# Kernel optimization log

Measured on AMD Instinct MI355X. Metric: run time of the kernel, lower is better.

The kernel has to match this reference:

```python
import jax, jax.numpy as jnp
import numpy as np

B, S, NGB, NG, DIM = 64, 4096, 13, 48, 3
NCH = [8, 8, 1]
NSHELLS = 8


def setup_inputs() -> dict:
    key = jax.random.key(0)
    ks = jax.random.split(key, 16)
    rng = np.random.default_rng(0)
    # valid row-wise permutations of the N_ngb neighbor slots per group op
    GnnPerms = jnp.asarray(np.argsort(rng.random((NG, NGB)), axis=1), dtype=jnp.int64)
    NNSites = jax.random.randint(ks[0], (NGB, S), 0, S, dtype=jnp.int64)
    SitesToShells = jax.random.randint(ks[1], (S,), 0, NSHELLS, dtype=jnp.int64)
    # block-diagonal (Ng*dim, Ng*dim) cartesian rotation blocks
    blk = rng.normal(size=(NG, DIM, DIM)).astype(np.float32) * 0.5
    gd = np.zeros((NG * DIM, NG * DIM), np.float32)
    for g in range(NG):
        gd[g * DIM:(g + 1) * DIM, g * DIM:(g + 1) * DIM] = blk[g]
    gdiags = jnp.asarray(gd)
    std = 0.2
    return {
        "InStates": jax.random.normal(ks[2], (B, 1, S), jnp.float32),
        "Psi0": jax.random.normal(ks[3], (NCH[0], 1, NGB), jnp.float32) * std,
        "bias0": jax.random.normal(ks[4], (NCH[0], 1), jnp.float32) * std,
        "Psi1": jax.random.normal(ks[5], (NCH[1], NCH[0], NGB), jnp.float32) * std,
        "bias1": jax.random.normal(ks[6], (NCH[1], 1), jnp.float32) * std,
        "Psi2": jax.random.normal(ks[7], (NCH[2], NCH[1], NGB), jnp.float32) * std,
        "bias2": jax.random.normal(ks[8], (NCH[2], 1), jnp.float32) * std,
        "wtVC": jax.random.normal(ks[9], (DIM, NGB), jnp.float32) * std,
        "ShellWeights": jax.random.normal(ks[10], (NSHELLS,), jnp.float32) * std,
        "gdiags": gdiags,
        "GnnPerms": GnnPerms,
        "NNSites": NNSites,
        "SitesToShells": SitesToShells,
    }


def _rearrange(x, NNSites):
    # x: (B, Nch, S) -> (B, Nch*N_ngb, S); subchannel j of channel c holds x[b, c, NNSites[j, s]]
    b, c, s = x.shape
    return x[:, :, NNSites].reshape(b, c * NGB, s)


def _gconv(x, W, b):
    # x: (B, NchIn*N_ngb, S); W: (NchOut, NchIn, N_ngb); b: (NchOut, 1)
    # group-rotated weights: GW[o, g, c*N_ngb+j] = W[o, c, GnnPerms[g, j]]
    GW = _gconv.GW_cache  # set per-call below via closure-free pattern; replaced in reference
    raise NotImplementedError


def reference(InStates, Psi0, bias0, Psi1, bias1, Psi2, bias2, wtVC,
              ShellWeights, gdiags, GnnPerms, NNSites, SitesToShells):
    act = jax.nn.softplus

    def gconv(x, W, b):
        # rotated weights: (NchOut, Ng, NchIn*N_ngb)
        GW = W[:, :, GnnPerms].transpose(0, 2, 1, 3).reshape(W.shape[0], NG, -1)
        h = jnp.einsum('ogk,bks->bogs', GW, x) + b[:, :, None]  # (B, NchOut, Ng, S)
        return act(h).mean(axis=2)                               # group-orbit average

    out = _rearrange(InStates, NNSites)
    for W, b in ((Psi0, bias0), (Psi1, bias1), (Psi2, bias2)):
        out = gconv(out, W, b)                 # (B, NchOut, S)
        out = _rearrange(out, NNSites)         # (B, NchOut*N_ngb, S)
    # vector channel: row g*dim+d of P is wtVC[d, GnnPerms[g]]
    P = wtVC[:, GnnPerms].transpose(1, 0, 2).reshape(NG * DIM, NGB)
    Wvc = gdiags @ P                           # (Ng*dim, N_ngb)
    v = jnp.einsum('kn,bns->bks', Wvc, out)    # (B, Ng*dim, S)
    v = v.reshape(-1, NG, DIM, out.shape[-1]).mean(axis=1)  # (B, dim, S)
    v = v * ShellWeights[SitesToShells]        # per-site shell weighting
    return v.sum(axis=2) / out.shape[-1]       # (B, dim)
```

## Files before the change

### kernel.cpp

```cpp
#include <hip/hip_runtime.h>
#include <hip/hip_bf16.h>

#define BATCH 64
#define SITES 4096
#define NGB 13
#define NGRP 48
#define SDIM 3

typedef __bf16 bf16x8 __attribute__((ext_vector_type(8)));
typedef float  f32x4  __attribute__((ext_vector_type(4)));

#define OFF_AVC  0
#define OFF_U    64
#define OFF_A0   67648
#define OFF_A1   2164800
#define OFF_PART 4261952
#define UW0H 0
#define UW0L 12288
#define UW1H 24576
#define UW1L 73728
#define UW2H 122880
#define UW2L 129024

__device__ __forceinline__ float softplus_f(float h) {
    return fmaxf(h, 0.f) + __logf(1.f + __expf(-fabsf(h)));
}

__global__ __launch_bounds__(256) void precompute_kernel(
    const float* __restrict__ Psi0, const float* __restrict__ Psi1,
    const float* __restrict__ Psi2, const float* __restrict__ wtVC,
    const float* __restrict__ gdiags, const int* __restrict__ perms,
    float* __restrict__ ws)
{
    float*  Avc = ws + OFF_AVC;
    __bf16* U   = (__bf16*)(ws + OFF_U);
    int t = blockIdx.x * 256 + threadIdx.x;
    if (t < 12288) {
        int k = t & 31, row = t >> 5;
        int o = row / NGRP, g = row - o * NGRP;
        float w = (k < NGB) ? Psi0[o * NGB + perms[g * NGB + k]] : 0.f;
        __bf16 hi = (__bf16)w;
        U[UW0H + t] = hi;
        U[UW0L + t] = (__bf16)(w - (float)hi);
    } else if (t < 61440) {
        int u = t - 12288;
        int k = u & 127, row = u >> 7;
        int o = row / NGRP, g = row - o * NGRP;
        float w = 0.f;
        if (k < 104) { int j = k >> 3, c = k & 7;
                       w = Psi1[(o * 8 + c) * NGB + perms[g * NGB + j]]; }
        __bf16 hi = (__bf16)w;
        U[UW1H + u] = hi;
        U[UW1L + u] = (__bf16)(w - (float)hi);
    } else if (t < 67584) {
        int u = t - 61440;
        int k = u & 127, g = u >> 7;
        float w = 0.f;
        if (k < 104) { int j = k >> 3, c = k & 7;
                       w = Psi2[c * NGB + perms[g * NGB + j]]; }
        __bf16 hi = (__bf16)w;
        U[UW2H + u] = hi;
        U[UW2L + u] = (__bf16)(w - (float)hi);
    } else if (t < 67584 + 39 * NGRP) {
        int t2 = t - 67584;
        int g = t2 % NGRP, u = t2 / NGRP;
        int d = u / NGB, n = u % NGB;
        const int row = g * SDIM + d;
        float s = 0.f;
        for (int k = 0; k < NGRP * SDIM; k++) {
            int g2 = k / SDIM, d2 = k - g2 * SDIM;
            float p = wtVC[d2 * NGB + perms[g2 * NGB + n]];
            s = fmaf(gdiags[row * (NGRP * SDIM) + k], p, s);
        }
        atomicAdd(&Avc[u], s * (1.f / 48.f));
    }
}

template<int NCIN, int NCTOT, int CT, int KPAD, int KSTR, int NWAVES, int NWN>
__global__ __launch_bounds__(NWAVES * 64) void layer_mfma(
    const float* __restrict__ prev,
    const __bf16* __restrict__ Wh,
    const __bf16* __restrict__ Wl,
    const float* __restrict__ bias,
    const int*   __restrict__ NN,
    float* __restrict__ out)
{
    constexpr int NTHR   = NWAVES * 64;
    constexpr int K      = NCIN * NGB;
    constexpr int M      = NCTOT * NGRP;
    constexpr int MTILES = M / 16, NTILES = CT / 16;
    constexpr int NWM    = NWAVES / NWN;
    constexpr int MT_W   = MTILES / NWM, NT_W = NTILES / NWN;
    constexpr int KT     = KPAD / 32;

    static_assert(MT_W * 16 == NGRP, "wave covers exactly one o");
    static_assert(NWM * MT_W == MTILES && NWN * NT_W == NTILES, "");
    static_assert((KPAD & 31) == 0 && (KSTR & 7) == 0, "");

    __shared__ __bf16 xh_lds[CT * KSTR];
    __shared__ __bf16 xl_lds[CT * KSTR];

    const int tid  = threadIdx.x;
    const int wave = tid >> 6, lane = tid & 63;
    const int m16  = lane & 15, quad = lane >> 4;

    const int b  = blockIdx.x / (SITES / CT);
    const int s0 = (blockIdx.x % (SITES / CT)) * CT;

    if constexpr (NCIN == 1) {
        for (int site = tid; site < NGB * CT; site += NTHR) {
            int j = site / CT, col = site % CT;
            int nn = NN[j * SITES + s0 + col];
            float v = prev[(size_t)b * SITES + nn];
            __bf16 hi = (__bf16)v;
            xh_lds[col * KSTR + j] = hi;
            xl_lds[col * KSTR + j] = (__bf16)(v - (float)hi);
        }
        for (int e = tid; e < CT * (KPAD - NGB); e += NTHR) {
            int col = e / (KPAD - NGB), p = e % (KPAD - NGB);
            xh_lds[col * KSTR + NGB + p] = (__bf16)0.f;
            xl_lds[col * KSTR + NGB + p] = (__bf16)0.f;
        }
    } else {
        for (int site = tid; site < NGB * CT; site += NTHR) {
            int j = site / CT, col = site % CT;
            int nn = NN[j * SITES + s0 + col];
            const float4* p4 = (const float4*)(prev + ((size_t)(b * SITES + nn)) * 8);
            float4 u0 = p4[0], u1 = p4[1];
            float v[8] = {u0.x, u0.y, u0.z, u0.w, u1.x, u1.y, u1.z, u1.w};
            bf16x8 hv, lv;
#pragma unroll
            for (int c = 0; c < 8; c++) {
                __bf16 hi = (__bf16)v[c];
                hv[c] = hi;
                lv[c] = (__bf16)(v[c] - (float)hi);
            }
            *(bf16x8*)(xh_lds + col * KSTR + j * 8) = hv;
            *(bf16x8*)(xl_lds + col * KSTR + j * 8) = lv;
        }
        const bf16x8 z8 = {};
        for (int e = tid; e < CT * 3; e += NTHR) {
            int col = e % CT, z = e / CT;
            *(bf16x8*)(xh_lds + col * KSTR + 104 + z * 8) = z8;
            *(bf16x8*)(xl_lds + col * KSTR + 104 + z * 8) = z8;
        }
    }
    __syncthreads();

    const int wave_mt0 = (wave / NWN) * MT_W;
    const int wave_nt0 = (wave % NWN) * NT_W;
    const int o_g      = (wave_mt0 * 16) / NGRP;

    f32x4 acc[MT_W][NT_W];
#pragma unroll
    for (int mt = 0; mt < MT_W; mt++)
#pragma unroll
        for (int nt = 0; nt < NT_W; nt++) acc[mt][nt] = (f32x4){0.f, 0.f, 0.f, 0.f};

#pragma unroll
    for (int kt = 0; kt < KT; kt++) {
        const int koff = kt * 32 + quad * 8;
        bf16x8 ah[MT_W], al[MT_W], bh[NT_W], bl[NT_W];
#pragma unroll
        for (int mt = 0; mt < MT_W; mt++) {
            int row = (wave_mt0 + mt) * 16 + m16;
            ah[mt] = *(const bf16x8*)(Wh + (size_t)row * KPAD + koff);
            al[mt] = *(const bf16x8*)(Wl + (size_t)row * KPAD + koff);
        }
#pragma unroll
        for (int nt = 0; nt < NT_W; nt++) {
            int cbase = ((wave_nt0 + nt) * 16 + m16) * KSTR + koff;
            bh[nt] = *(const bf16x8*)(xh_lds + cbase);
            bl[nt] = *(const bf16x8*)(xl_lds + cbase);
        }
#pragma unroll
        for (int mt = 0; mt < MT_W; mt++)
#pragma unroll
            for (int nt = 0; nt < NT_W; nt++) {
                acc[mt][nt] = __builtin_amdgcn_mfma_f32_16x16x32_bf16(
                    ah[mt], bh[nt], acc[mt][nt], 0, 0, 0);
                acc[mt][nt] = __builtin_amdgcn_mfma_f32_16x16x32_bf16(
                    al[mt], bh[nt], acc[mt][nt], 0, 0, 0);
                acc[mt][nt] = __builtin_amdgcn_mfma_f32_16x16x32_bf16(
                    ah[mt], bl[nt], acc[mt][nt], 0, 0, 0);
            }
    }

    const float bo = bias[o_g];
#pragma unroll
    for (int nt = 0; nt < NT_W; nt++) {
        float s = 0.f;
#pragma unroll
        for (int mt = 0; mt < MT_W; mt++)
#pragma unroll
            for (int r = 0; r < 4; r++)
                s += softplus_f(acc[mt][nt][r] + bo);
        s += __shfl_xor(s, 16);
        s += __shfl_xor(s, 32);
        if (quad == 0)
            out[((size_t)(b * SITES + s0 + (wave_nt0 + nt) * 16 + m16)) * NCTOT + o_g]
                = s * (1.f / 48.f);
    }
}

__global__ __launch_bounds__(256) void reduce_a(
    const float* __restrict__ A2, const int* __restrict__ NN,
    const int* __restrict__ s2sh, const float* __restrict__ sw,
    const float* __restrict__ Avc, float* __restrict__ partial)
{
    const int b = blockIdx.x >> 4;
    const int chunk = blockIdx.x & 15;
    const int tid = threadIdx.x;
    const int s = (chunk << 8) + tid;
    const float* a = A2 + (size_t)b * SITES;

    float y0 = 0.f, y1 = 0.f, y2 = 0.f;
#pragma unroll
    for (int n = 0; n < NGB; n++) {
        float v = a[NN[n * SITES + s]];
        y0 = fmaf(Avc[n],           v, y0);
        y1 = fmaf(Avc[NGB + n],     v, y1);
        y2 = fmaf(Avc[2 * NGB + n], v, y2);
    }
    const float wgt = sw[s2sh[s]];
    y0 *= wgt; y1 *= wgt; y2 *= wgt;

    __shared__ float red[3][256];
    red[0][tid] = y0; red[1][tid] = y1; red[2][tid] = y2;
    __syncthreads();
    for (int st = 128; st > 0; st >>= 1) {
        if (tid < st) {
            red[0][tid] += red[0][tid + st];
            red[1][tid] += red[1][tid + st];
            red[2][tid] += red[2][tid + st];
        }
        __syncthreads();
    }
    if (tid < 3) partial[(b * 16 + chunk) * 3 + tid] = red[tid][0];
}

__global__ __launch_bounds__(256) void reduce_b(
    const float* __restrict__ partial, float* __restrict__ out)
{
    int t = threadIdx.x;
    if (t < BATCH * 3) {
        int b = t / 3, d = t - b * 3;
        float s = 0.f;
        for (int c = 0; c < 16; c++) s += partial[(b * 16 + c) * 3 + d];
        out[t] = s * (1.f / (float)SITES);
    }
}

extern "C" void kernel_launch(void* const* d_in, const int* in_sizes, int n_in,
                              void* d_out, int out_size, void* d_ws, size_t ws_size,
                              hipStream_t stream)
{
    const float* InStates = (const float*)d_in[0];
    const float* Psi0     = (const float*)d_in[1];
    const float* bias0    = (const float*)d_in[2];
    const float* Psi1     = (const float*)d_in[3];
    const float* bias1    = (const float*)d_in[4];
    const float* Psi2     = (const float*)d_in[5];
    const float* bias2    = (const float*)d_in[6];
    const float* wtVC     = (const float*)d_in[7];
    const float* ShellW   = (const float*)d_in[8];
    const float* gdiags   = (const float*)d_in[9];
    const int*   GnnPerms = (const int*)d_in[10];
    const int*   NNSites  = (const int*)d_in[11];
    const int*   S2Sh     = (const int*)d_in[12];

    float*  ws   = (float*)d_ws;
    float*  Avc  = ws + OFF_AVC;
    __bf16* U    = (__bf16*)(ws + OFF_U);
    float*  A0   = ws + OFF_A0;
    float*  A1   = ws + OFF_A1;
    float*  A2   = ws + OFF_A0;
    float*  PART = ws + OFF_PART;

    float* out = (float*)d_out;

    hipMemsetAsync(Avc, 0, 39 * sizeof(float), stream);
    precompute_kernel<<<272, 256, 0, stream>>>(Psi0, Psi1, Psi2, wtVC, gdiags,
                                               GnnPerms, ws);

    layer_mfma<1, 8, 64, 32, 40, 8, 1><<<BATCH * (SITES / 64), 512, 0, stream>>>(
        InStates, U + UW0H, U + UW0L, bias0, NNSites, A0);
    layer_mfma<8, 8, 64, 128, 136, 8, 1><<<BATCH * (SITES / 64), 512, 0, stream>>>(
        A0, U + UW1H, U + UW1L, bias1, NNSites, A1);
    layer_mfma<8, 1, 64, 128, 136, 4, 4><<<BATCH * (SITES / 64), 256, 0, stream>>>(
        A1, U + UW2H, U + UW2L, bias2, NNSites, A2);

    reduce_a<<<BATCH * 16, 256, 0, stream>>>(A2, NNSites, S2Sh, ShellW, Avc, PART);
    reduce_b<<<1, 256, 0, stream>>>(PART, out);
}
```

Measured before the change: 372.6 us.

## Make layer kernels persistent over site chunks with double-buffered LDS gather prefetch

Each block of the layer kernels now handles 8 consecutive 64-site chunks instead of one. The neighbour gather for the next chunk is issued into registers before the MFMA loop and written to a second LDS buffer afterwards, with NN indices loaded two chunks ahead. This aims to hide gather latency behind MFMA work and to amortise block setup and zero-padding. In exchange it launches 8x fewer blocks, which may reduce parallelism across CUs, adds register pressure for the prefetched data, and doubles LDS use.

```diff
diff --git a/kernel.cpp b/kernel.cpp
--- a/kernel.cpp
+++ b/kernel.cpp
@@ -76,8 +76,9 @@
     }
 }
 
-template<int NCIN, int NCTOT, int CT, int KPAD, int KSTR, int NWAVES, int NWN>
-__global__ __launch_bounds__(NWAVES * 64) void layer_mfma(
+template<int NCIN, int NCTOT, int CT, int KPAD, int KSTR, int NWAVES, int NWN,
+         int CHUNKS>
+__global__ __launch_bounds__(NWAVES * 64, 4) void layer_mfma(
     const float* __restrict__ prev,
     const __bf16* __restrict__ Wh,
     const __bf16* __restrict__ Wl,
@@ -86,120 +87,209 @@
     float* __restrict__ out)
 {
     constexpr int NTHR   = NWAVES * 64;
-    constexpr int K      = NCIN * NGB;
     constexpr int M      = NCTOT * NGRP;
     constexpr int MTILES = M / 16, NTILES = CT / 16;
     constexpr int NWM    = NWAVES / NWN;
     constexpr int MT_W   = MTILES / NWM, NT_W = NTILES / NWN;
     constexpr int KT     = KPAD / 32;
+    constexpr int GS     = NGB * CT;
+    constexpr int SPT    = (GS + NTHR - 1) / NTHR;
+    constexpr int CPB    = SITES / CT;
+    constexpr int BUF    = CT * KSTR;
 
     static_assert(MT_W * 16 == NGRP, "wave covers exactly one o");
     static_assert(NWM * MT_W == MTILES && NWN * NT_W == NTILES, "");
     static_assert((KPAD & 31) == 0 && (KSTR & 7) == 0, "");
-
-    __shared__ __bf16 xh_lds[CT * KSTR];
-    __shared__ __bf16 xl_lds[CT * KSTR];
+    static_assert(CPB % CHUNKS == 0, "block stays within one batch");
+
+    __shared__ __bf16 xh_lds[2 * BUF];
+    __shared__ __bf16 xl_lds[2 * BUF];
 
     const int tid  = threadIdx.x;
     const int wave = tid >> 6, lane = tid & 63;
     const int m16  = lane & 15, quad = lane >> 4;
 
-    const int b  = blockIdx.x / (SITES / CT);
-    const int s0 = (blockIdx.x % (SITES / CT)) * CT;
+    const int chunk0 = blockIdx.x * CHUNKS;
+    const int b      = chunk0 / CPB;
+    const int s0base = (chunk0 % CPB) * CT;
+
+    int sj[SPT], scol[SPT];
+    bool sv[SPT];
+#pragma unroll
+    for (int i = 0; i < SPT; i++) {
+        int site = tid + i * NTHR;
+        sv[i] = (site < GS);
+        int ss = sv[i] ? site : 0;
+        sj[i] = ss / CT;
+        scol[i] = ss % CT;
+    }
 
     if constexpr (NCIN == 1) {
-        for (int site = tid; site < NGB * CT; site += NTHR) {
-            int j = site / CT, col = site % CT;
-            int nn = NN[j * SITES + s0 + col];
+        for (int e = tid; e < 2 * CT * (KPAD - NGB); e += NTHR) {
+            int buf = e / (CT * (KPAD - NGB));
+            int r   = e % (CT * (KPAD - NGB));
+            int col = r / (KPAD - NGB), p = r % (KPAD - NGB);
+            xh_lds[buf * BUF + col * KSTR + NGB + p] = (__bf16)0.f;
+            xl_lds[buf * BUF + col * KSTR + NGB + p] = (__bf16)0.f;
+        }
+    } else {
+        const bf16x8 z8 = {};
+        for (int e = tid; e < 2 * CT * 3; e += NTHR) {
+            int buf = e / (CT * 3);
+            int r   = e % (CT * 3);
+            int col = r % CT, z = r / CT;
+            *(bf16x8*)(xh_lds + buf * BUF + col * KSTR + 104 + z * 8) = z8;
+            *(bf16x8*)(xl_lds + buf * BUF + col * KSTR + 104 + z * 8) = z8;
+        }
+    }
+
+#pragma unroll
+    for (int i = 0; i < SPT; i++) if (sv[i]) {
+        int nn = NN[sj[i] * SITES + s0base + scol[i]];
+        if constexpr (NCIN == 1) {
             float v = prev[(size_t)b * SITES + nn];
             __bf16 hi = (__bf16)v;
-            xh_lds[col * KSTR + j] = hi;
-            xl_lds[col * KSTR + j] = (__bf16)(v - (float)hi);
-        }
-        for (int e = tid; e < CT * (KPAD - NGB); e += NTHR) {
-            int col = e / (KPAD - NGB), p = e % (KPAD - NGB);
-            xh_lds[col * KSTR + NGB + p] = (__bf16)0.f;
-            xl_lds[col * KSTR + NGB + p] = (__bf16)0.f;
-        }
-    } else {
-        for (int site = tid; site < NGB * CT; site += NTHR) {
-            int j = site / CT, col = site % CT;
-            int nn = NN[j * SITES + s0 + col];
+            xh_lds[scol[i] * KSTR + sj[i]] = hi;
+            xl_lds[scol[i] * KSTR + sj[i]] = (__bf16)(v - (float)hi);
+        } else {
             const float4* p4 = (const float4*)(prev + ((size_t)(b * SITES + nn)) * 8);
             float4 u0 = p4[0], u1 = p4[1];
             float v[8] = {u0.x, u0.y, u0.z, u0.w, u1.x, u1.y, u1.z, u1.w};
             bf16x8 hv, lv;
 #pragma unroll
-            for (int c = 0; c < 8; c++) {
-                __bf16 hi = (__bf16)v[c];
-                hv[c] = hi;
-                lv[c] = (__bf16)(v[c] - (float)hi);
-            }
-            *(bf16x8*)(xh_lds + col * KSTR + j * 8) = hv;
-            *(bf16x8*)(xl_lds + col * KSTR + j * 8) = lv;
-        }
-        const bf16x8 z8 = {};
-        for (int e = tid; e < CT * 3; e += NTHR) {
-            int col = e % CT, z = e / CT;
-            *(bf16x8*)(xh_lds + col * KSTR + 104 + z * 8) = z8;
-            *(bf16x8*)(xl_lds + col * KSTR + 104 + z * 8) = z8;
-        }
+            for (int c8 = 0; c8 < 8; c8++) {
+                __bf16 hi = (__bf16)v[c8];
+                hv[c8] = hi;
+                lv[c8] = (__bf16)(v[c8] - (float)hi);
+            }
+            *(bf16x8*)(xh_lds + scol[i] * KSTR + sj[i] * 8) = hv;
+            *(bf16x8*)(xl_lds + scol[i] * KSTR + sj[i] * 8) = lv;
+        }
+    }
+
+    int nnA[SPT];
+    if (CHUNKS > 1) {
+        const int s1 = s0base + CT;
+#pragma unroll
+        for (int i = 0; i < SPT; i++)
+            nnA[i] = sv[i] ? NN[sj[i] * SITES + s1 + scol[i]] : 0;
     }
     __syncthreads();
 
     const int wave_mt0 = (wave / NWN) * MT_W;
     const int wave_nt0 = (wave % NWN) * NT_W;
     const int o_g      = (wave_mt0 * 16) / NGRP;
-
-    f32x4 acc[MT_W][NT_W];
-#pragma unroll
-    for (int mt = 0; mt < MT_W; mt++)
-#pragma unroll
-        for (int nt = 0; nt < NT_W; nt++) acc[mt][nt] = (f32x4){0.f, 0.f, 0.f, 0.f};
-
-#pragma unroll
-    for (int kt = 0; kt < KT; kt++) {
-        const int koff = kt * 32 + quad * 8;
-        bf16x8 ah[MT_W], al[MT_W], bh[NT_W], bl[NT_W];
-#pragma unroll
-        for (int mt = 0; mt < MT_W; mt++) {
-            int row = (wave_mt0 + mt) * 16 + m16;
-            ah[mt] = *(const bf16x8*)(Wh + (size_t)row * KPAD + koff);
-            al[mt] = *(const bf16x8*)(Wl + (size_t)row * KPAD + koff);
-        }
+    const float bo     = bias[o_g];
+
+#pragma unroll 1
+    for (int c = 0; c < CHUNKS; c++) {
+        const int cur = c & 1;
+
+        float4 ga[SPT], gb[SPT];
+        float  g1[SPT];
+        if (c + 1 < CHUNKS) {
+#pragma unroll
+            for (int i = 0; i < SPT; i++) if (sv[i]) {
+                if constexpr (NCIN == 1) {
+                    g1[i] = prev[(size_t)b * SITES + nnA[i]];
+                } else {
+                    const float4* p4 =
+                        (const float4*)(prev + ((size_t)(b * SITES + nnA[i])) * 8);
+                    ga[i] = p4[0];
+                    gb[i] = p4[1];
+                }
+            }
+        }
+        int nnB[SPT];
+        if (c + 2 < CHUNKS) {
+            const int s2 = s0base + (c + 2) * CT;
+#pragma unroll
+            for (int i = 0; i < SPT; i++)
+                nnB[i] = sv[i] ? NN[sj[i] * SITES + s2 + scol[i]] : 0;
+        }
+
+        const __bf16* xh = xh_lds + cur * BUF;
+        const __bf16* xl = xl_lds + cur * BUF;
+
+        f32x4 acc[MT_W][NT_W];
+#pragma unroll
+        for (int mt = 0; mt < MT_W; mt++)
+#pragma unroll
+            for (int nt = 0; nt < NT_W; nt++) acc[mt][nt] = (f32x4){0.f, 0.f, 0.f, 0.f};
+
+#pragma unroll
+        for (int kt = 0; kt < KT; kt++) {
+            const int koff = kt * 32 + quad * 8;
+            bf16x8 ah[MT_W], al[MT_W], bh[NT_W], bl[NT_W];
+#pragma unroll
+            for (int mt = 0; mt < MT_W; mt++) {
+                int row = (wave_mt0 + mt) * 16 + m16;
+                ah[mt] = *(const bf16x8*)(Wh + (size_t)row * KPAD + koff);
+                al[mt] = *(const bf16x8*)(Wl + (size_t)row * KPAD + koff);
+            }
+#pragma unroll
+            for (int nt = 0; nt < NT_W; nt++) {
+                int cbase = ((wave_nt0 + nt) * 16 + m16) * KSTR + koff;
+                bh[nt] = *(const bf16x8*)(xh + cbase);
+                bl[nt] = *(const bf16x8*)(xl + cbase);
+            }
+#pragma unroll
+            for (int mt = 0; mt < MT_W; mt++)
+#pragma unroll
+                for (int nt = 0; nt < NT_W; nt++) {
+                    acc[mt][nt] = __builtin_amdgcn_mfma_f32_16x16x32_bf16(
+                        ah[mt], bh[nt], acc[mt][nt], 0, 0, 0);
+                    acc[mt][nt] = __builtin_amdgcn_mfma_f32_16x16x32_bf16(
+                        al[mt], bh[nt], acc[mt][nt], 0, 0, 0);
+                    acc[mt][nt] = __builtin_amdgcn_mfma_f32_16x16x32_bf16(
+                        ah[mt], bl[nt], acc[mt][nt], 0, 0, 0);
+                }
+        }
+
+        const int s0c = s0base + c * CT;
 #pragma unroll
         for (int nt = 0; nt < NT_W; nt++) {
-            int cbase = ((wave_nt0 + nt) * 16 + m16) * KSTR + koff;
-            bh[nt] = *(const bf16x8*)(xh_lds + cbase);
-            bl[nt] = *(const bf16x8*)(xl_lds + cbase);
-        }
-#pragma unroll
-        for (int mt = 0; mt < MT_W; mt++)
-#pragma unroll
-            for (int nt = 0; nt < NT_W; nt++) {
-                acc[mt][nt] = __builtin_amdgcn_mfma_f32_16x16x32_bf16(
-                    ah[mt], bh[nt], acc[mt][nt], 0, 0, 0);
-                acc[mt][nt] = __builtin_amdgcn_mfma_f32_16x16x32_bf16(
-                    al[mt], bh[nt], acc[mt][nt], 0, 0, 0);
-                acc[mt][nt] = __builtin_amdgcn_mfma_f32_16x16x32_bf16(
-                    ah[mt], bl[nt], acc[mt][nt], 0, 0, 0);
-            }
-    }
-
-    const float bo = bias[o_g];
-#pragma unroll
-    for (int nt = 0; nt < NT_W; nt++) {
-        float s = 0.f;
-#pragma unroll
-        for (int mt = 0; mt < MT_W; mt++)
-#pragma unroll
-            for (int r = 0; r < 4; r++)
-                s += softplus_f(acc[mt][nt][r] + bo);
-        s += __shfl_xor(s, 16);
-        s += __shfl_xor(s, 32);
-        if (quad == 0)
-            out[((size_t)(b * SITES + s0 + (wave_nt0 + nt) * 16 + m16)) * NCTOT + o_g]
-                = s * (1.f / 48.f);
+            float s = 0.f;
+#pragma unroll
+            for (int mt = 0; mt < MT_W; mt++)
+#pragma unroll
+                for (int r = 0; r < 4; r++)
+                    s += softplus_f(acc[mt][nt][r] + bo);
+            s += __shfl_xor(s, 16);
+            s += __shfl_xor(s, 32);
+            if (quad == 0)
+                out[((size_t)(b * SITES + s0c + (wave_nt0 + nt) * 16 + m16)) * NCTOT + o_g]
+                    = s * (1.f / 48.f);
+        }
+
+        if (c + 1 < CHUNKS) {
+            __bf16* dh = xh_lds + (cur ^ 1) * BUF;
+            __bf16* dl = xl_lds + (cur ^ 1) * BUF;
+#pragma unroll
+            for (int i = 0; i < SPT; i++) if (sv[i]) {
+                if constexpr (NCIN == 1) {
+                    float v = g1[i];
+                    __bf16 hi = (__bf16)v;
+                    dh[scol[i] * KSTR + sj[i]] = hi;
+                    dl[scol[i] * KSTR + sj[i]] = (__bf16)(v - (float)hi);
+                } else {
+                    float v[8] = {ga[i].x, ga[i].y, ga[i].z, ga[i].w,
+                                  gb[i].x, gb[i].y, gb[i].z, gb[i].w};
+                    bf16x8 hv, lv;
+#pragma unroll
+                    for (int c8 = 0; c8 < 8; c8++) {
+                        __bf16 hi = (__bf16)v[c8];
+                        hv[c8] = hi;
+                        lv[c8] = (__bf16)(v[c8] - (float)hi);
+                    }
+                    *(bf16x8*)(dh + scol[i] * KSTR + sj[i] * 8) = hv;
+                    *(bf16x8*)(dl + scol[i] * KSTR + sj[i] * 8) = lv;
+                }
+            }
+#pragma unroll
+            for (int i = 0; i < SPT; i++) nnA[i] = nnB[i];
+        }
+        __syncthreads();
     }
 }
 
@@ -283,11 +373,14 @@
     precompute_kernel<<<272, 256, 0, stream>>>(Psi0, Psi1, Psi2, wtVC, gdiags,
                                                GnnPerms, ws);
 
-    layer_mfma<1, 8, 64, 32, 40, 8, 1><<<BATCH * (SITES / 64), 512, 0, stream>>>(
+    constexpr int CHUNKS = 8;
+    constexpr int NBLK   = BATCH * (SITES / 64) / CHUNKS;
+
+    layer_mfma<1, 8, 64, 32, 40, 8, 1, CHUNKS><<<NBLK, 512, 0, stream>>>(
         InStates, U + UW0H, U + UW0L, bias0, NNSites, A0);
-    layer_mfma<8, 8, 64, 128, 136, 8, 1><<<BATCH * (SITES / 64), 512, 0, stream>>>(
+    layer_mfma<8, 8, 64, 128, 136, 8, 1, CHUNKS><<<NBLK, 512, 0, stream>>>(
         A0, U + UW1H, U + UW1L, bias1, NNSites, A1);
-    layer_mfma<8, 1, 64, 128, 136, 4, 4><<<BATCH * (SITES / 64), 256, 0, stream>>>(
+    layer_mfma<8, 1, 64, 128, 136, 4, 4, CHUNKS><<<NBLK, 256, 0, stream>>>(
         A1, U + UW2H, U + UW2L, bias2, NNSites, A2);
 
     reduce_a<<<BATCH * 16, 256, 0, stream>>>(A2, NNSites, S2Sh, ShellW, Avc, PART);
```

New measurement: 414.3 us. 1.11x slower.
